# Kernel optimization log

Hardware: AMD Instinct MI355X
Metric: run time of the kernel (lower is better)

Reference implementation:

```python
import jax, jax.numpy as jnp
import numpy as np

# ---- db4 filters (pywt conventions: dec_lo = rec_lo[::-1], rec_hi = qmf(rec_lo)) ----
F = 8  # db4 filter length
_rec_lo = np.array([0.23037781330885523, 0.7148465705525415, 0.6308807679295904,
                    -0.027983769416983849, -0.18703481171888114, 0.030841381835986965,
                    0.032883011666982945, -0.010597401784997278], dtype=np.float32)
_rec_hi = _rec_lo[::-1].copy()
_rec_hi[1::2] *= -1.0
REC_LO = jnp.asarray(_rec_lo)
REC_HI = jnp.asarray(_rec_hi)

MAX_LEVEL = 9  # pywt.dwt_max_level(4096, 8)


def _conv1d(x, kernel, stride=1, padding='VALID', lhs_dilation=None):
    # x: [B, L] -> correlation (XLA conv does NOT flip the kernel)
    out = jax.lax.conv_general_dilated(
        x[:, None, :], kernel[None, None, :],
        window_strides=(stride,), padding=padding,
        lhs_dilation=lhs_dilation,
        dimension_numbers=('NCH', 'OIH', 'NCH'))
    return out[:, 0, :]


def dwt(x):
    # pywt.dwt(x, 'db4', mode='symmetric'):
    # cA = np.convolve(sym_ext(x, F-1), dec_lo, 'valid')[1::2]
    # convolution with dec filter == correlation with rec filter (its reverse)
    ext = jnp.pad(x, ((0, 0), (F - 1, F - 1)), mode='symmetric')[:, 1:]
    return _conv1d(ext, REC_LO, stride=2), _conv1d(ext, REC_HI, stride=2)


def idwt(ca, cd):
    # pywt.idwt: zero-upsample coeffs, full convolution with rec filters, trim edges
    n = ca.shape[1]
    pad = ((F - 1, F - 1),)
    out = (_conv1d(ca, REC_LO[::-1], padding=pad, lhs_dilation=(2,)) +
           _conv1d(cd, REC_HI[::-1], padding=pad, lhs_dilation=(2,)))
    return out[:, F - 2:2 * n]  # output length = 2n - F + 2


def wavelet_features(x1):
    # Faithful to WaveletDWTLayer stack + WaveletParsingLayer: at each level k>=2,
    # reconstruct with details of levels k and k-1 only (others zeroed), with
    # pywt.waverec's trim-by-one rule; concatenate the 8 full-length reconstructions.
    a = x1
    cds, recs = [], []
    for level in range(1, MAX_LEVEL + 1):
        a, d = dwt(a)
        if level >= 2:
            r = idwt(jnp.zeros_like(d), d)
            for j in range(level - 2, -1, -1):
                dj = cds[j] if j == level - 2 else jnp.zeros_like(cds[j])
                if r.shape[1] == dj.shape[1] + 1:  # waverec trim rule
                    r = r[:, :-1]
                r = idwt(r, dj)
            recs.append(r)  # [B, signal_length]
        cds.append(d)
    return jnp.concatenate(recs, axis=1)  # [B, signal_length*(MAX_LEVEL-1)]


def reference(x1, x2, x3, W0, b0, W1, b1, W2, b2):
    # x2/x3 are placeholders in the original module (overwritten by layers 1/2)
    h = wavelet_features(x1)
    for W, b in ((W0, b0), (W1, b1), (W2, b2)):
        h = jax.nn.relu(h) @ W.T + b
    return h


def setup_inputs() -> dict:
    key = jax.random.key(0)
    ks = jax.random.split(key, 4)
    B, N = 2048, 4096
    D_IN, H1, H2, OUT = 32768, 181, 13, 10
    return {
        'x1': jax.random.normal(ks[0], (B, N), jnp.float32),
        'x2': jnp.zeros((B, 1, 8), jnp.float32),
        'x3': jnp.zeros((B, 1, 8), jnp.float32),
        'W0': jax.random.normal(ks[1], (H1, D_IN), jnp.float32) / np.float32(np.sqrt(D_IN)),
        'b0': jnp.zeros((H1,), jnp.float32),
        'W1': jax.random.normal(ks[2], (H2, H1), jnp.float32) / np.float32(np.sqrt(H1)),
        'b1': jnp.zeros((H2,), jnp.float32),
        'W2': jax.random.normal(ks[3], (OUT, H2), jnp.float32) / np.float32(np.sqrt(H2)),
        'b2': jnp.zeros((OUT,), jnp.float32),
    }
```

## Files before the change

kernel.cpp:

```cpp
#include <hip/hip_runtime.h>
#include <hip/hip_bf16.h>


typedef _Float16 f16x8 __attribute__((ext_vector_type(8)));
typedef _Float16 f16x4v __attribute__((ext_vector_type(4)));
typedef float f32x4 __attribute__((ext_vector_type(4)));

#define WV_THREADS 256
#define DROW 4160
#define NSPLIT 32
#define KCHUNK 1024

#define L0 0.23037781330885523f
#define L1 0.7148465705525415f
#define L2f 0.6308807679295904f
#define L3 -0.02798376941698385f
#define L4 -0.18703481171888114f
#define L5 0.030841381835986965f
#define L6 0.032883011666982945f
#define L7 -0.010597401784997278f

#define H0 -0.010597401784997278f
#define H1 -0.032883011666982945f
#define H2 0.030841381835986965f
#define H3 0.18703481171888114f
#define H4 -0.02798376941698385f
#define H5 -0.6308807679295904f
#define H6 0.7148465705525415f
#define H7 -0.23037781330885523f

__constant__ constexpr int cNL[10]   = {4096, 2051, 1029, 518, 262, 134, 70, 38, 22, 14};
__constant__ constexpr int cDOFF[10] = {0, 0, 2052, 3084, 3604, 3868, 4004, 4076, 4116, 4140};

__device__ __forceinline__ int ext_idx(int j, int n) {
  return (j < 6) ? (5 - j) : ((j < n + 6) ? (j - 6) : (2 * n + 5 - j));
}

__device__ __forceinline__ void dwt2(const float* a, float* anext, float* d,
                                     int n, int m, bool store_a) {
  const int ng = (m + 1) >> 1;
  for (int g = threadIdx.x; g < ng; g += WV_THREADS) {
    float w[10];
    if (g >= 2 && 4 * g + 9 <= n + 5) {
      const float2* af = (const float2*)a + (2 * g - 3);
      float2 b0 = af[0], b1 = af[1], b2 = af[2], b3 = af[3], b4 = af[4];
      w[0] = b0.x; w[1] = b0.y; w[2] = b1.x; w[3] = b1.y; w[4] = b2.x;
      w[5] = b2.y; w[6] = b3.x; w[7] = b3.y; w[8] = b4.x; w[9] = b4.y;
    } else {
#pragma unroll
      for (int q = 0; q < 10; ++q) {
        int j = 4 * g + q;
        int jm = n + 12;
        if (j > jm) j = jm;
        w[q] = a[ext_idx(j, n)];
      }
    }
    float sl0 = w[0]*L0 + w[1]*L1 + w[2]*L2f + w[3]*L3 + w[4]*L4 + w[5]*L5 + w[6]*L6 + w[7]*L7;
    float sh0 = w[0]*H0 + w[1]*H1 + w[2]*H2  + w[3]*H3 + w[4]*H4 + w[5]*H5 + w[6]*H6 + w[7]*H7;
    float sl1 = w[2]*L0 + w[3]*L1 + w[4]*L2f + w[5]*L3 + w[6]*L4 + w[7]*L5 + w[8]*L6 + w[9]*L7;
    float sh1 = w[2]*H0 + w[3]*H1 + w[4]*H2  + w[5]*H3 + w[6]*H4 + w[7]*H5 + w[8]*H6 + w[9]*H7;
    if (2 * g + 1 < m) {
      if (store_a) *(float2*)(anext + 2 * g) = make_float2(sl0, sl1);
      *(float2*)(d + 2 * g) = make_float2(sh0, sh1);
    } else {
      if (store_a) anext[2 * g] = sl0;
      d[2 * g] = sh0;
    }
  }
}

template <bool HAS_CA, bool HAS_CD, bool FINAL, int DLEN>
__device__ __forceinline__ void idwt4t(const float* ca, const float* cd,
                                       float* outl, _Float16* outg) {
  constexpr int npair = DLEN - 3;
  constexpr int ng4 = (npair + 3) >> 2;
#pragma unroll
  for (int t0 = 0; t0 < ng4; t0 += WV_THREADS) {
    const int t = t0 + (int)threadIdx.x;
    if (t < ng4) {
      float w[8], v[8];
      if (HAS_CA) {
        float4 A4 = ((const float4*)ca)[t];
        float4 B4 = ((const float4*)ca)[t + 1];
        w[0]=A4.x; w[1]=A4.y; w[2]=A4.z; w[3]=A4.w;
        w[4]=B4.x; w[5]=B4.y; w[6]=B4.z; w[7]=B4.w;
      }
      if (HAS_CD) {
        float4 C4 = ((const float4*)cd)[t];
        float4 D4 = ((const float4*)cd)[t + 1];
        v[0]=C4.x; v[1]=C4.y; v[2]=C4.z; v[3]=C4.w;
        v[4]=D4.x; v[5]=D4.y; v[6]=D4.z; v[7]=D4.w;
      }
      float e[4], o[4];
#pragma unroll
      for (int q = 0; q < 4; ++q) {
        float eq = 0.f, oq = 0.f;
        if (HAS_CA) {
          eq = w[q+3]*L0 + w[q+2]*L2f + w[q+1]*L4 + w[q]*L6;
          oq = w[q+3]*L1 + w[q+2]*L3  + w[q+1]*L5 + w[q]*L7;
        }
        if (HAS_CD) {
          eq += v[q+3]*H0 + v[q+2]*H2 + v[q+1]*H4 + v[q]*H6;
          oq += v[q+3]*H1 + v[q+2]*H3 + v[q+1]*H5 + v[q]*H7;
        }
        e[q] = eq; o[q] = oq;
      }
      if (FINAL) {
        f16x8 h;
        h[0] = (_Float16)fmaxf(e[0], 0.f); h[1] = (_Float16)fmaxf(o[0], 0.f);
        h[2] = (_Float16)fmaxf(e[1], 0.f); h[3] = (_Float16)fmaxf(o[1], 0.f);
        h[4] = (_Float16)fmaxf(e[2], 0.f); h[5] = (_Float16)fmaxf(o[2], 0.f);
        h[6] = (_Float16)fmaxf(e[3], 0.f); h[7] = (_Float16)fmaxf(o[3], 0.f);
        *(f16x8*)(outg + 8 * t) = h;
      } else {
        if (4 * t + 3 < npair) {
          ((float4*)(outl + 8 * t))[0] = make_float4(e[0], o[0], e[1], o[1]);
          ((float4*)(outl + 8 * t))[1] = make_float4(e[2], o[2], e[3], o[3]);
        } else {
#pragma unroll
          for (int q = 0; q < 4; ++q)
            if (4 * t + q < npair)
              *(float2*)(outl + 8 * t + 2 * q) = make_float2(e[q], o[q]);
        }
      }
    }
  }
}

template <int L>
__device__ __forceinline__ void synth_cascade(const float* dr, _Float16* og,
                                              float* s1, float* s2) {
  idwt4t<false, true, false, cNL[L]>(nullptr, dr + cDOFF[L], s1, nullptr);
  __syncthreads();
  float* cur = s1;
  float* nxt = s2;
  if constexpr (L >= 3) {
    idwt4t<true, true, false, cNL[L - 1]>(cur, dr + cDOFF[L - 1], nxt, nullptr);
    __syncthreads();
    float* t = cur; cur = nxt; nxt = t;
  }
#define NOCD_STEP(DL)                                             \
  {                                                               \
    idwt4t<true, false, false, DL>(cur, nullptr, nxt, nullptr);   \
    __syncthreads();                                              \
    float* t = cur; cur = nxt; nxt = t;                           \
  }
  if constexpr (L >= 9) NOCD_STEP(cNL[7])
  if constexpr (L >= 8) NOCD_STEP(cNL[6])
  if constexpr (L >= 7) NOCD_STEP(cNL[5])
  if constexpr (L >= 6) NOCD_STEP(cNL[4])
  if constexpr (L >= 5) NOCD_STEP(cNL[3])
  if constexpr (L >= 4) NOCD_STEP(cNL[2])
#undef NOCD_STEP
  idwt4t<true, (L == 2), true, 2051>(cur, (L == 2) ? dr + cDOFF[1] : nullptr,
                                     nullptr, og);
}

__global__ __launch_bounds__(WV_THREADS) void wv_analysis_cvt(
    const float* __restrict__ x, float* __restrict__ dG,
    const float* __restrict__ W0, _Float16* __restrict__ Bw) {
  __shared__ float r1[4104];
  __shared__ float r2[2056];
  const int tid = threadIdx.x;

  if (blockIdx.x >= 2048) {
    size_t i = ((size_t)(blockIdx.x - 2048) * 256 + tid) * 4;
    int rowc = (int)(i >> 15);
    f16x4v h;
    if (rowc < 181) {
      const float4 v = *(const float4*)(W0 + i);
      h[0] = (_Float16)v.x; h[1] = (_Float16)v.y;
      h[2] = (_Float16)v.z; h[3] = (_Float16)v.w;
    } else {
      h[0] = (_Float16)0.f; h[1] = (_Float16)0.f;
      h[2] = (_Float16)0.f; h[3] = (_Float16)0.f;
    }
    *(f16x4v*)(Bw + i) = h;
    return;
  }

  const int NLa[10]  = {4096, 2051, 1029, 518, 262, 134, 70, 38, 22, 14};
  const int DOFF[10] = {0, 0, 2052, 3084, 3604, 3868, 4004, 4076, 4116, 4140};
  const int LOFF[10] = {0, 0, 1036, 520, 2068, 1040, 2332, 1176, 2404, 1216};
  const int row = blockIdx.x;

  const float4* xr = (const float4*)(x + (size_t)row * 4096);
  for (int i = tid; i < 1024; i += WV_THREADS) ((float4*)r1)[i] = xr[i];
  __syncthreads();

  float* dr = dG + (size_t)row * DROW;
  dwt2(r1, r2, dr + DOFF[1], NLa[0], NLa[1], true);
  __syncthreads();
  const float* ap = r2;
  float* an = r1;
  for (int lev = 2; lev <= 9; ++lev) {
    float* dbuf = ((lev & 1) ? r2 : r1) + LOFF[lev];
    dwt2(ap, an, dbuf, NLa[lev - 1], NLa[lev], lev < 9);
    __syncthreads();
    const float* t = ap; ap = an; an = (float*)t;
  }
  for (int lev = 2; lev <= 9; ++lev) {
    const float* src = ((lev & 1) ? r2 : r1) + LOFF[lev];
    float* dst = dr + DOFF[lev];
    const int n = NLa[lev];
    for (int i = 2 * tid; i + 1 < n; i += 2 * WV_THREADS)
      *(float2*)(dst + i) = *(const float2*)(src + i);
    if ((n & 1) && tid == 0) dst[n - 1] = src[n - 1];
  }
}

__global__ __launch_bounds__(WV_THREADS, 6) void wv_synth(
    const float* __restrict__ dG, _Float16* __restrict__ A) {
  __shared__ float s1[2052];
  __shared__ float s2[2052];
  const int row = blockIdx.x;
  const float* dr = dG + (size_t)row * DROW;
  _Float16* og = A + (size_t)row * 32768 + (size_t)blockIdx.y * 4096;
  switch (blockIdx.y) {
    case 0: synth_cascade<2>(dr, og, s1, s2); break;
    case 1: synth_cascade<3>(dr, og, s1, s2); break;
    case 2: synth_cascade<4>(dr, og, s1, s2); break;
    case 3: synth_cascade<5>(dr, og, s1, s2); break;
    case 4: synth_cascade<6>(dr, og, s1, s2); break;
    case 5: synth_cascade<7>(dr, og, s1, s2); break;
    case 6: synth_cascade<8>(dr, og, s1, s2); break;
    default: synth_cascade<9>(dr, og, s1, s2); break;
  }
}

__device__ __forceinline__ void load_lds16(const void* g, void* l) {
  __builtin_amdgcn_global_load_lds((__attribute__((address_space(1))) unsigned int*)g,
                                   (__attribute__((address_space(3))) unsigned int*)l,
                                   16, 0, 0);
}

__global__ __launch_bounds__(256, 2) void gemm_kernel(
    const _Float16* __restrict__ A, const _Float16* __restrict__ Bw,
    float* __restrict__ P) {
  __shared__ _Float16 As[128 * 64];
  __shared__ _Float16 Bs[192 * 64];
  const int tid = threadIdx.x;
  const int lane = tid & 63;
  const int wave = tid >> 6;
  const int m0 = blockIdx.x * 128;
  const int k_idx = blockIdx.y;
  const int k0 = k_idx * KCHUNK;

  f32x4 acc[2][12];
#pragma unroll
  for (int mt = 0; mt < 2; ++mt)
#pragma unroll
    for (int nt = 0; nt < 12; ++nt) acc[mt][nt] = (f32x4){0.f, 0.f, 0.f, 0.f};

  for (int ks = 0; ks < (KCHUNK >> 6); ++ks) {
    const int kbase = k0 + (ks << 6);
    __syncthreads();
#pragma unroll
    for (int t = 0; t < 4; ++t) {
      int g = ((wave * 4 + t) << 6) + lane;
      int r = g >> 3, cs = g & 7;
      const _Float16* gp = A + (size_t)(m0 + r) * 32768 + kbase + ((cs ^ (r & 7)) << 3);
      load_lds16(gp, (char*)As + (size_t)((wave * 4 + t) << 10));
    }
#pragma unroll
    for (int t = 0; t < 6; ++t) {
      int g = ((wave * 6 + t) << 6) + lane;
      int r = g >> 3, cs = g & 7;
      const _Float16* gp = Bw + (size_t)r * 32768 + kbase + ((cs ^ (r & 7)) << 3);
      load_lds16(gp, (char*)Bs + (size_t)((wave * 6 + t) << 10));
    }
    __syncthreads();
#pragma unroll
    for (int kk = 0; kk < 2; ++kk) {
      const int chunk = kk * 4 + (lane >> 4);
      f16x8 af[2];
#pragma unroll
      for (int mt = 0; mt < 2; ++mt) {
        int r = wave * 32 + mt * 16 + (lane & 15);
        af[mt] = *(const f16x8*)(As + r * 64 + ((chunk ^ (r & 7)) << 3));
      }
#pragma unroll
      for (int nt = 0; nt < 12; ++nt) {
        int rb = nt * 16 + (lane & 15);
        f16x8 bf = *(const f16x8*)(Bs + rb * 64 + ((chunk ^ (rb & 7)) << 3));
        acc[0][nt] = __builtin_amdgcn_mfma_f32_16x16x32_f16(af[0], bf, acc[0][nt], 0, 0, 0);
        acc[1][nt] = __builtin_amdgcn_mfma_f32_16x16x32_f16(af[1], bf, acc[1][nt], 0, 0, 0);
      }
    }
  }
  float* Pp = P + ((size_t)k_idx * 2048 + m0) * 192;
#pragma unroll
  for (int mt = 0; mt < 2; ++mt)
#pragma unroll
    for (int nt = 0; nt < 12; ++nt)
#pragma unroll
      for (int r4 = 0; r4 < 4; ++r4) {
        int rr = wave * 32 + mt * 16 + ((lane >> 4) << 2) + r4;
        int cc = nt * 16 + (lane & 15);
        Pp[(size_t)rr * 192 + cc] = acc[mt][nt][r4];
      }
}

__global__ __launch_bounds__(256) void mlp_kernel(
    const float* __restrict__ P, const float* __restrict__ b0,
    const float* __restrict__ W1, const float* __restrict__ b1,
    const float* __restrict__ W2, const float* __restrict__ b2,
    float* __restrict__ out) {
  __shared__ float part[4][193];
  __shared__ float h1[192];
  __shared__ float h2[13];
  const int row = blockIdx.x;
  const int t = threadIdx.x;
  const int g = t >> 6;
  const int l = t & 63;

  float a0 = 0.f, a1 = 0.f, a2 = 0.f;
  for (int si = 0; si < NSPLIT / 4; ++si) {
    int s = g + (si << 2);
    const float* Pr = P + ((size_t)s * 2048 + row) * 192;
    a0 += Pr[l]; a1 += Pr[64 + l]; a2 += Pr[128 + l];
  }
  part[g][l] = a0; part[g][64 + l] = a1; part[g][128 + l] = a2;
  __syncthreads();

  if (t < 192) {
    float v = part[0][t] + part[1][t] + part[2][t] + part[3][t];
    h1[t] = (t < 181) ? fmaxf(v + b0[t], 0.f) : 0.f;
  }
  __syncthreads();

#pragma unroll
  for (int r = 0; r < 4; ++r) {
    int j = g + (r << 2);
    if (j < 13) {
      float v = 0.f;
#pragma unroll
      for (int q = 0; q < 3; ++q) {
        int n = l + (q << 6);
        if (n < 181) v += h1[n] * W1[j * 181 + n];
      }
      for (int off = 32; off >= 1; off >>= 1) v += __shfl_down(v, off);
      if (l == 0) h2[j] = fmaxf(v + b1[j], 0.f);
    }
  }
  __syncthreads();

  if (t < 10) {
    float c = b2[t];
#pragma unroll
    for (int j = 0; j < 13; ++j) c += h2[j] * W2[t * 13 + j];
    out[(size_t)row * 10 + t] = c;
  }
}

extern "C" void kernel_launch(void* const* d_in, const int* in_sizes, int n_in,
                              void* d_out, int out_size, void* d_ws, size_t ws_size,
                              hipStream_t stream) {
  const float* x1 = (const float*)d_in[0];
  const float* W0 = (const float*)d_in[3];
  const float* b0 = (const float*)d_in[4];
  const float* W1 = (const float*)d_in[5];
  const float* b1 = (const float*)d_in[6];
  const float* W2 = (const float*)d_in[7];
  const float* b2 = (const float*)d_in[8];
  float* out = (float*)d_out;

  char* ws = (char*)d_ws;
  const size_t A_BYTES = (size_t)2048 * 32768 * 2;
  const size_t B_BYTES = (size_t)192 * 32768 * 2;
  _Float16* Afeat = (_Float16*)ws;
  _Float16* Bw = (_Float16*)(ws + A_BYTES);
  float* Dq = (float*)(ws + A_BYTES + B_BYTES);
  float* P = (float*)(ws + A_BYTES + B_BYTES);

  wv_analysis_cvt<<<2048 + 6144, WV_THREADS, 0, stream>>>(x1, Dq, W0, Bw);
  dim3 sg(2048, 8);
  wv_synth<<<sg, WV_THREADS, 0, stream>>>(Dq, Afeat);
  dim3 gg(16, NSPLIT);
  gemm_kernel<<<gg, 256, 0, stream>>>(Afeat, Bw, P);
  mlp_kernel<<<2048, 256, 0, stream>>>(P, b0, W1, b1, W2, b2, out);
}
```

Measured before the change: 218.6 us.

## Fuse wavelet synthesis cascade into per-thread register chains and double-buffer GEMM

The multi-level inverse DWT cascade, which bounced between two shared-memory buffers with a barrier per level, is replaced by per-thread register chains. Each thread reconstructs its output segment directly from the detail coefficients, using at most one swizzled LDS handoff and one barrier. Separately, the GEMM moves to 512-thread blocks with 256-row M tiles and double-buffered LDS staging, so the next K-slice is loaded while MFMAs run on the current one. The new synthesis code does redundant overlapping computation per thread and uses more registers, and the larger GEMM block uses more LDS, which can lower occupancy.

```diff
diff --git a/kernel.cpp b/kernel.cpp
--- a/kernel.cpp
+++ b/kernel.cpp
@@ -10,6 +10,7 @@
 #define DROW 4160
 #define NSPLIT 32
 #define KCHUNK 1024
+#define GEMM_BM 256
 
 #define L0 0.23037781330885523f
 #define L1 0.7148465705525415f
@@ -69,91 +70,172 @@
   }
 }
 
-template <bool HAS_CA, bool HAS_CD, bool FINAL, int DLEN>
-__device__ __forceinline__ void idwt4t(const float* ca, const float* cd,
-                                       float* outl, _Float16* outg) {
-  constexpr int npair = DLEN - 3;
-  constexpr int ng4 = (npair + 3) >> 2;
-#pragma unroll
-  for (int t0 = 0; t0 < ng4; t0 += WV_THREADS) {
-    const int t = t0 + (int)threadIdx.x;
-    if (t < ng4) {
-      float w[8], v[8];
-      if (HAS_CA) {
-        float4 A4 = ((const float4*)ca)[t];
-        float4 B4 = ((const float4*)ca)[t + 1];
-        w[0]=A4.x; w[1]=A4.y; w[2]=A4.z; w[3]=A4.w;
-        w[4]=B4.x; w[5]=B4.y; w[6]=B4.z; w[7]=B4.w;
-      }
-      if (HAS_CD) {
-        float4 C4 = ((const float4*)cd)[t];
-        float4 D4 = ((const float4*)cd)[t + 1];
-        v[0]=C4.x; v[1]=C4.y; v[2]=C4.z; v[3]=C4.w;
-        v[4]=D4.x; v[5]=D4.y; v[6]=D4.z; v[7]=D4.w;
-      }
-      float e[4], o[4];
-#pragma unroll
-      for (int q = 0; q < 4; ++q) {
-        float eq = 0.f, oq = 0.f;
-        if (HAS_CA) {
-          eq = w[q+3]*L0 + w[q+2]*L2f + w[q+1]*L4 + w[q]*L6;
-          oq = w[q+3]*L1 + w[q+2]*L3  + w[q+1]*L5 + w[q]*L7;
-        }
-        if (HAS_CD) {
-          eq += v[q+3]*H0 + v[q+2]*H2 + v[q+1]*H4 + v[q]*H6;
-          oq += v[q+3]*H1 + v[q+2]*H3 + v[q+1]*H5 + v[q]*H7;
-        }
-        e[q] = eq; o[q] = oq;
-      }
-      if (FINAL) {
-        f16x8 h;
-        h[0] = (_Float16)fmaxf(e[0], 0.f); h[1] = (_Float16)fmaxf(o[0], 0.f);
-        h[2] = (_Float16)fmaxf(e[1], 0.f); h[3] = (_Float16)fmaxf(o[1], 0.f);
-        h[4] = (_Float16)fmaxf(e[2], 0.f); h[5] = (_Float16)fmaxf(o[2], 0.f);
-        h[6] = (_Float16)fmaxf(e[3], 0.f); h[7] = (_Float16)fmaxf(o[3], 0.f);
-        *(f16x8*)(outg + 8 * t) = h;
-      } else {
-        if (4 * t + 3 < npair) {
-          ((float4*)(outl + 8 * t))[0] = make_float4(e[0], o[0], e[1], o[1]);
-          ((float4*)(outl + 8 * t))[1] = make_float4(e[2], o[2], e[3], o[3]);
-        } else {
-#pragma unroll
-          for (int q = 0; q < 4; ++q)
-            if (4 * t + q < npair)
-              *(float2*)(outl + 8 * t + 2 * q) = make_float2(e[q], o[q]);
-        }
-      }
-    }
-  }
-}
-
-template <int L>
-__device__ __forceinline__ void synth_cascade(const float* dr, _Float16* og,
-                                              float* s1, float* s2) {
-  idwt4t<false, true, false, cNL[L]>(nullptr, dr + cDOFF[L], s1, nullptr);
-  __syncthreads();
-  float* cur = s1;
-  float* nxt = s2;
-  if constexpr (L >= 3) {
-    idwt4t<true, true, false, cNL[L - 1]>(cur, dr + cDOFF[L - 1], nxt, nullptr);
-    __syncthreads();
-    float* t = cur; cur = nxt; nxt = t;
-  }
-#define NOCD_STEP(DL)                                             \
-  {                                                               \
-    idwt4t<true, false, false, DL>(cur, nullptr, nxt, nullptr);   \
-    __syncthreads();                                              \
-    float* t = cur; cur = nxt; nxt = t;                           \
-  }
-  if constexpr (L >= 9) NOCD_STEP(cNL[7])
-  if constexpr (L >= 8) NOCD_STEP(cNL[6])
-  if constexpr (L >= 7) NOCD_STEP(cNL[5])
-  if constexpr (L >= 6) NOCD_STEP(cNL[4])
-  if constexpr (L >= 5) NOCD_STEP(cNL[3])
-  if constexpr (L >= 4) NOCD_STEP(cNL[2])
-#undef NOCD_STEP
-  idwt4t<true, (L == 2), true, 2051>(cur, (L == 2) ? dr + cDOFF[1] : nullptr,
-                                     nullptr, og);
+#define SWZ(u) ((u) ^ (((u) >> 3) & 7))
+__device__ __forceinline__ const float4* lds4c(const float* b, int s) {
+  return (const float4*)b + SWZ(s);
+}
+__device__ __forceinline__ float4* lds4(float* b, int s) {
+  return (float4*)b + SWZ(s);
+}
+
+template <int NP>
+__device__ __forceinline__ void lvlL(const float* a, float* v) {
+#pragma unroll
+  for (int q = 0; q < NP; ++q) {
+    v[2*q]   = a[q+3]*L0 + a[q+2]*L2f + a[q+1]*L4 + a[q]*L6;
+    v[2*q+1] = a[q+3]*L1 + a[q+2]*L3  + a[q+1]*L5 + a[q]*L7;
+  }
+}
+template <int NP>
+__device__ __forceinline__ void lvlH(const float* d, float* v) {
+#pragma unroll
+  for (int q = 0; q < NP; ++q) {
+    v[2*q]   = d[q+3]*H0 + d[q+2]*H2 + d[q+1]*H4 + d[q]*H6;
+    v[2*q+1] = d[q+3]*H1 + d[q+2]*H3 + d[q+1]*H5 + d[q]*H7;
+  }
+}
+template <int NP>
+__device__ __forceinline__ void lvlLH(const float* a, const float* d, float* v) {
+#pragma unroll
+  for (int q = 0; q < NP; ++q) {
+    v[2*q]   = a[q+3]*L0 + a[q+2]*L2f + a[q+1]*L4 + a[q]*L6
+             + d[q+3]*H0 + d[q+2]*H2  + d[q+1]*H4 + d[q]*H6;
+    v[2*q+1] = a[q+3]*L1 + a[q+2]*L3  + a[q+1]*L5 + a[q]*L7
+             + d[q+3]*H1 + d[q+2]*H3  + d[q+1]*H5 + d[q]*H7;
+  }
+}
+
+__device__ __forceinline__ void g7(const float* p, int s, float* w) {
+#pragma unroll
+  for (int i = 0; i < 7; ++i) w[i] = p[s + i];
+}
+__device__ __forceinline__ void g8f2(const float* p, int s, float* w) {
+#pragma unroll
+  for (int i = 0; i < 4; ++i) {
+    float2 v = *(const float2*)(p + s + 2 * i);
+    w[2*i] = v.x; w[2*i+1] = v.y;
+  }
+}
+__device__ __forceinline__ void g12f4(const float* p, int s, float* w) {
+#pragma unroll
+  for (int i = 0; i < 3; ++i) {
+    float4 v = *(const float4*)(p + s + 4 * i);
+    w[4*i] = v.x; w[4*i+1] = v.y; w[4*i+2] = v.z; w[4*i+3] = v.w;
+  }
+}
+
+__device__ __forceinline__ void store16(_Float16* outg, int t, const float* v) {
+  f16x8 h0, h1;
+#pragma unroll
+  for (int i = 0; i < 8; ++i) h0[i] = (_Float16)fmaxf(v[i], 0.f);
+#pragma unroll
+  for (int i = 0; i < 8; ++i) h1[i] = (_Float16)fmaxf(v[8 + i], 0.f);
+  *(f16x8*)(outg + 16 * t) = h0;
+  *(f16x8*)(outg + 16 * t + 8) = h1;
+}
+
+__device__ __forceinline__ void fin2(const float* d2, const float* d1, _Float16* og) {
+  const int t = threadIdx.x;
+  float dw[12];  g12f4(d2, 4 * t, dw);
+  float mid[12]; lvlH<6>(dw, mid);
+  float d1w[12]; g12f4(d1, 8 * t, d1w);
+  float v[16];   lvlLH<8>(mid, d1w, v);
+  store16(og, t, v);
+}
+
+__device__ __forceinline__ void fin3(const float* d3, const float* d2, _Float16* og) {
+  const int t = threadIdx.x;
+  float dw[8];   g8f2(d3, 2 * t, dw);
+  float v0[10];  lvlH<5>(dw, v0);
+  float d2w[12]; g12f4(d2, 4 * t, d2w);
+  float v1[12];  lvlLH<6>(v0, d2w, v1);
+  float v[16];   lvlL<8>(v1, v);
+  store16(og, t, v);
+}
+
+__device__ __forceinline__ void fin4(const float* d4, const float* d3, _Float16* og) {
+  const int t = threadIdx.x;
+  float dw[7];   g7(d4, t, dw);
+  float v0[8];   lvlH<4>(dw, v0);
+  float d3w[8];  g8f2(d3, 2 * t, d3w);
+  float v1[10];  lvlLH<5>(v0, d3w, v1);
+  float v2[12];  lvlL<6>(v1, v2);
+  float v[16];   lvlL<8>(v2, v);
+  store16(og, t, v);
+}
+
+template <int NG>
+__device__ __forceinline__ void chainA4(const float* dL, const float* dm, float* outl) {
+  const int t = threadIdx.x;
+  if (t >= NG) return;
+  float dw[7];  g7(dL, t, dw);
+  float v0[8];  lvlH<4>(dw, v0);
+  float dmw[8]; g8f2(dm, 2 * t, dmw);
+  float v1[10]; lvlLH<5>(v0, dmw, v1);
+  float v2[12]; lvlL<6>(v1, v2);
+  float v[16];  lvlL<8>(v2, v);
+#pragma unroll
+  for (int j = 0; j < 4; ++j)
+    *lds4(outl, 4 * t + j) = make_float4(v[4*j], v[4*j+1], v[4*j+2], v[4*j+3]);
+}
+
+template <int NG>
+__device__ __forceinline__ void chainA6(const float* dL, const float* dm, float* outl) {
+  const int t = threadIdx.x;
+  if (t >= NG) return;
+  const int s1 = t >> 1, s2 = s1 >> 1;
+  float dw[7];  g7(dL, s2, dw);
+  float u0[8];  lvlH<4>(dw, u0);
+  float dmw[7]; g7(dm, s1, dmw);
+  float u1[8];  lvlLH<4>(u0 + (s1 & 1), dmw, u1);
+  float u2[8];  lvlL<4>(u1 + (t & 1), u2);
+  float u3[10]; lvlL<5>(u2, u3);
+  float u4[12]; lvlL<6>(u3, u4);
+  float v[16];  lvlL<8>(u4, v);
+#pragma unroll
+  for (int j = 0; j < 4; ++j)
+    *lds4(outl, 4 * t + j) = make_float4(v[4*j], v[4*j+1], v[4*j+2], v[4*j+3]);
+}
+
+template <int NG>
+__device__ __forceinline__ void chainA8(const float* dL, const float* dm, float* outl) {
+  const int t = threadIdx.x;
+  if (t >= NG) return;
+  const int s1 = t >> 1, s2 = s1 >> 1, s3 = s2 >> 1, s4 = s3 >> 1;
+  float dw[7];  g7(dL, s4, dw);
+  float u0[8];  lvlH<4>(dw, u0);
+  float dmw[7]; g7(dm, s3, dmw);
+  float u1[8];  lvlLH<4>(u0 + (s3 & 1), dmw, u1);
+  float u2[8];  lvlL<4>(u1 + (s2 & 1), u2);
+  float u3[8];  lvlL<4>(u2 + (s1 & 1), u3);
+  float u4[8];  lvlL<4>(u3 + (t & 1), u4);
+  float u5[10]; lvlL<5>(u4, u5);
+  float u6[12]; lvlL<6>(u5, u6);
+  float v[16];  lvlL<8>(u6, v);
+#pragma unroll
+  for (int j = 0; j < 4; ++j)
+    *lds4(outl, 4 * t + j) = make_float4(v[4*j], v[4*j+1], v[4*j+2], v[4*j+3]);
+}
+
+__device__ __forceinline__ void finalB(const float* s, _Float16* og) {
+  const int t = threadIdx.x;
+  float w[12];
+  float4 a = *lds4c(s, 2*t), b = *lds4c(s, 2*t + 1), c = *lds4c(s, 2*t + 2);
+  w[0]=a.x; w[1]=a.y; w[2]=a.z; w[3]=a.w; w[4]=b.x; w[5]=b.y; w[6]=b.z; w[7]=b.w;
+  w[8]=c.x; w[9]=c.y; w[10]=c.z; w[11]=c.w;
+  float v[16]; lvlL<8>(w, v);
+  store16(og, t, v);
+}
+
+__device__ __forceinline__ void finpairB(const float* s, _Float16* og) {
+  const int t = threadIdx.x;
+  float w[12];
+  float4 a = *lds4c(s, t), b = *lds4c(s, t + 1), c = *lds4c(s, t + 2);
+  w[0]=a.x; w[1]=a.y; w[2]=a.z; w[3]=a.w; w[4]=b.x; w[5]=b.y; w[6]=b.z; w[7]=b.w;
+  w[8]=c.x; w[9]=c.y; w[10]=c.z; w[11]=c.w;
+  float r[12]; lvlL<6>(w, r);
+  float v[16]; lvlL<8>(r, v);
+  store16(og, t, v);
 }
 
 __global__ __launch_bounds__(WV_THREADS) void wv_analysis_cvt(
@@ -211,20 +293,24 @@
 
 __global__ __launch_bounds__(WV_THREADS, 6) void wv_synth(
     const float* __restrict__ dG, _Float16* __restrict__ A) {
-  __shared__ float s1[2052];
-  __shared__ float s2[2052];
+  __shared__ alignas(16) float s1[2080];
   const int row = blockIdx.x;
   const float* dr = dG + (size_t)row * DROW;
   _Float16* og = A + (size_t)row * 32768 + (size_t)blockIdx.y * 4096;
   switch (blockIdx.y) {
-    case 0: synth_cascade<2>(dr, og, s1, s2); break;
-    case 1: synth_cascade<3>(dr, og, s1, s2); break;
-    case 2: synth_cascade<4>(dr, og, s1, s2); break;
-    case 3: synth_cascade<5>(dr, og, s1, s2); break;
-    case 4: synth_cascade<6>(dr, og, s1, s2); break;
-    case 5: synth_cascade<7>(dr, og, s1, s2); break;
-    case 6: synth_cascade<8>(dr, og, s1, s2); break;
-    default: synth_cascade<9>(dr, og, s1, s2); break;
+    case 0: fin2(dr + cDOFF[2], dr + cDOFF[1], og); break;
+    case 1: fin3(dr + cDOFF[3], dr + cDOFF[2], og); break;
+    case 2: fin4(dr + cDOFF[4], dr + cDOFF[3], og); break;
+    case 3: chainA4<129>(dr + cDOFF[5], dr + cDOFF[4], s1); __syncthreads();
+            finalB(s1, og); break;
+    case 4: chainA4<65>(dr + cDOFF[6], dr + cDOFF[5], s1); __syncthreads();
+            finpairB(s1, og); break;
+    case 5: chainA6<129>(dr + cDOFF[7], dr + cDOFF[6], s1); __syncthreads();
+            finalB(s1, og); break;
+    case 6: chainA6<65>(dr + cDOFF[8], dr + cDOFF[7], s1); __syncthreads();
+            finpairB(s1, og); break;
+    default: chainA8<129>(dr + cDOFF[9], dr + cDOFF[8], s1); __syncthreads();
+            finalB(s1, og); break;
   }
 }
 
@@ -234,15 +320,15 @@
                                    16, 0, 0);
 }
 
-__global__ __launch_bounds__(256, 2) void gemm_kernel(
+__global__ __launch_bounds__(512, 2) void gemm_kernel(
     const _Float16* __restrict__ A, const _Float16* __restrict__ Bw,
     float* __restrict__ P) {
-  __shared__ _Float16 As[128 * 64];
-  __shared__ _Float16 Bs[192 * 64];
+  __shared__ _Float16 As[2][GEMM_BM * 64];
+  __shared__ _Float16 Bs[2][192 * 64];
   const int tid = threadIdx.x;
   const int lane = tid & 63;
   const int wave = tid >> 6;
-  const int m0 = blockIdx.x * 128;
+  const int m0 = blockIdx.x * GEMM_BM;
   const int k_idx = blockIdx.y;
   const int k0 = k_idx * KCHUNK;
 
@@ -252,24 +338,32 @@
 #pragma unroll
     for (int nt = 0; nt < 12; ++nt) acc[mt][nt] = (f32x4){0.f, 0.f, 0.f, 0.f};
 
-  for (int ks = 0; ks < (KCHUNK >> 6); ++ks) {
+  auto stage = [&](int ks, int b) {
     const int kbase = k0 + (ks << 6);
-    __syncthreads();
 #pragma unroll
     for (int t = 0; t < 4; ++t) {
-      int g = ((wave * 4 + t) << 6) + lane;
+      int c = wave * 4 + t;
+      int g = (c << 6) + lane;
       int r = g >> 3, cs = g & 7;
       const _Float16* gp = A + (size_t)(m0 + r) * 32768 + kbase + ((cs ^ (r & 7)) << 3);
-      load_lds16(gp, (char*)As + (size_t)((wave * 4 + t) << 10));
-    }
-#pragma unroll
-    for (int t = 0; t < 6; ++t) {
-      int g = ((wave * 6 + t) << 6) + lane;
+      load_lds16(gp, (char*)As[b] + ((size_t)c << 10));
+    }
+#pragma unroll
+    for (int t = 0; t < 3; ++t) {
+      int c = wave * 3 + t;
+      int g = (c << 6) + lane;
       int r = g >> 3, cs = g & 7;
       const _Float16* gp = Bw + (size_t)r * 32768 + kbase + ((cs ^ (r & 7)) << 3);
-      load_lds16(gp, (char*)Bs + (size_t)((wave * 6 + t) << 10));
-    }
-    __syncthreads();
+      load_lds16(gp, (char*)Bs[b] + ((size_t)c << 10));
+    }
+  };
+
+  stage(0, 0);
+  __syncthreads();
+
+  for (int ks = 0; ks < (KCHUNK >> 6); ++ks) {
+    const int cur = ks & 1;
+    if (ks + 1 < (KCHUNK >> 6)) stage(ks + 1, cur ^ 1);
 #pragma unroll
     for (int kk = 0; kk < 2; ++kk) {
       const int chunk = kk * 4 + (lane >> 4);
@@ -277,17 +371,19 @@
 #pragma unroll
       for (int mt = 0; mt < 2; ++mt) {
         int r = wave * 32 + mt * 16 + (lane & 15);
-        af[mt] = *(const f16x8*)(As + r * 64 + ((chunk ^ (r & 7)) << 3));
+        af[mt] = *(const f16x8*)(As[cur] + r * 64 + ((chunk ^ (r & 7)) << 3));
       }
 #pragma unroll
       for (int nt = 0; nt < 12; ++nt) {
         int rb = nt * 16 + (lane & 15);
-        f16x8 bf = *(const f16x8*)(Bs + rb * 64 + ((chunk ^ (rb & 7)) << 3));
+        f16x8 bf = *(const f16x8*)(Bs[cur] + rb * 64 + ((chunk ^ (rb & 7)) << 3));
         acc[0][nt] = __builtin_amdgcn_mfma_f32_16x16x32_f16(af[0], bf, acc[0][nt], 0, 0, 0);
         acc[1][nt] = __builtin_amdgcn_mfma_f32_16x16x32_f16(af[1], bf, acc[1][nt], 0, 0, 0);
       }
     }
-  }
+    __syncthreads();
+  }
+
   float* Pp = P + ((size_t)k_idx * 2048 + m0) * 192;
 #pragma unroll
   for (int mt = 0; mt < 2; ++mt)
@@ -376,7 +472,7 @@
   wv_analysis_cvt<<<2048 + 6144, WV_THREADS, 0, stream>>>(x1, Dq, W0, Bw);
   dim3 sg(2048, 8);
   wv_synth<<<sg, WV_THREADS, 0, stream>>>(Dq, Afeat);
-  dim3 gg(16, NSPLIT);
-  gemm_kernel<<<gg, 256, 0, stream>>>(Afeat, Bw, P);
+  dim3 gg(2048 / GEMM_BM, NSPLIT);
+  gemm_kernel<<<gg, 512, 0, stream>>>(Afeat, Bw, P);
   mlp_kernel<<<2048, 256, 0, stream>>>(P, b0, W1, b1, W2, b2, out);
 }
```

Measured after the change: 237.5 us. 1.09x slower.
